# Kernel tuning notes

Measured on AMD Instinct MI355X. Metric: run time of the kernel, lower is better.

## Reference

```python
import jax, jax.numpy as jnp
import numpy as np

B, M = 512, 32          # graphs, atoms per graph
N = B * M               # 16384 nodes
F_IN, H, L = 16, 128, 2 # input feat, hidden, n interaction layers
CUTOFF = 1.0
BOX = 2.0               # side of position box -> avg degree ~16 at r=1


def _glorot(k, shape):
    fan_in = shape[-2]
    return jax.random.normal(k, shape, dtype=jnp.float32) / np.sqrt(fan_in)


def setup_inputs():
    key = jax.random.key(0)
    ks = jax.random.split(key, 12)
    return {
        "h": jax.random.normal(ks[0], (N, F_IN), dtype=jnp.float32),
        "x": jax.random.uniform(ks[1], (N, 3), dtype=jnp.float32) * BOX,
        "batch": jnp.repeat(jnp.arange(B, dtype=jnp.int32), M),
        "W_in": _glorot(ks[2], (F_IN, H)), "b_in": jnp.zeros((H,), jnp.float32),
        "We1": _glorot(ks[3], (L, 2 * H + 1, H)), "be1": jnp.zeros((L, H), jnp.float32),
        "We2": _glorot(ks[4], (L, H, H)), "be2": jnp.zeros((L, H), jnp.float32),
        "Wh1": _glorot(ks[5], (L, 2 * H, H)), "bh1": jnp.zeros((L, H), jnp.float32),
        "Wh2": _glorot(ks[6], (L, H, H)), "bh2": jnp.zeros((L, H), jnp.float32),
        "W_out": _glorot(ks[7], (H, H)), "b_out": jnp.zeros((H,), jnp.float32),
        "Wn1": _glorot(ks[8], (H, H)), "bn1": jnp.zeros((H,), jnp.float32),
        "Wn2": _glorot(ks[9], (H, 1)), "bn2": jnp.zeros((1,), jnp.float32),
    }


def reference(h, x, batch, W_in, b_in, We1, be1, We2, be2, Wh1, bh1, Wh2, bh2, W_out, b_out, Wn1, bn1, Wn2, bn2):
    # radius graph within each molecule, fixed-shape dense mask [B,M,M]
    xg = x.reshape(B, M, 3)
    diff = xg[:, :, None, :] - xg[:, None, :, :]                 # [B,M,M,3]
    d2 = jnp.sum(diff * diff, axis=-1)                            # [B,M,M]
    adj = (d2 < CUTOFF * CUTOFF) & (~jnp.eye(M, dtype=bool))      # no self-loops

    hg = (h @ W_in + b_in).reshape(B, M, H)                       # embedding_in
    for l in range(L):  # sake_conv interaction layers
        Wa, Wb, wd = We1[l, :H], We1[l, H:2 * H], We1[l, 2 * H]
        mi = jnp.einsum('bmh,hk->bmk', hg, Wa)
        mj = jnp.einsum('bmh,hk->bmk', hg, Wb)
        # edge message phi_e([h_i, h_j, ||x_i-x_j||^2])
        m = jax.nn.silu(mi[:, :, None, :] + mj[:, None, :, :] + d2[..., None] * wd + be1[l])
        m = jax.nn.silu(jnp.einsum('bijh,hk->bijk', m, We2[l]) + be2[l])
        m = jnp.where(adj[..., None], m, 0.0)
        agg = jnp.sum(m, axis=2)                                  # scatter-add over neighbors j
        # node update phi_h([h_i, m_i]) with residual
        u = jax.nn.silu(jnp.einsum('bmh,hk->bmk', hg, Wh1[l, :H])
                        + jnp.einsum('bmh,hk->bmk', agg, Wh1[l, H:]) + bh1[l])
        hg = hg + jnp.einsum('bmh,hk->bmk', u, Wh2[l]) + bh2[l]

    ho = hg.reshape(N, H) @ W_out + b_out                         # embedding_out
    e = jax.nn.silu(ho @ Wn1 + bn1) @ Wn2 + bn2                   # energy_network -> [N,1]
    out = jax.ops.segment_sum(e, batch, num_segments=B)           # per-graph energy pooling
    return out.squeeze()
```

## Files before the change

### kernel.cpp

```cpp
#include <hip/hip_runtime.h>
#include <hip/hip_bf16.h>


#define NB 512

typedef __bf16 bf16x8 __attribute__((ext_vector_type(8)));
typedef __bf16 bf16x2 __attribute__((ext_vector_type(2)));
typedef float f32x4 __attribute__((ext_vector_type(4)));

__device__ __forceinline__ unsigned short f2bf(float f) {
    unsigned int u = __float_as_uint(f);
    u = u + 0x7FFFu + ((u >> 16) & 1u);
    return (unsigned short)(u >> 16);
}
__device__ __forceinline__ unsigned int packbf(float lo, float hi) {
    bf16x2 t;
    t.x = (__bf16)lo;
    t.y = (__bf16)hi;
    return __builtin_bit_cast(unsigned int, t);
}
__device__ __forceinline__ float bflo(unsigned int u) { return __uint_as_float(u << 16); }
__device__ __forceinline__ float bfhi(unsigned int u) { return __uint_as_float(u & 0xffff0000u); }
__device__ __forceinline__ float silu_f(float v) {
    return v * __builtin_amdgcn_rcpf(1.0f + __expf(-v));
}

__global__ __launch_bounds__(256) void prep_weights(
        const float* __restrict__ We1, const float* __restrict__ We2,
        const float* __restrict__ Wh1, const float* __restrict__ Wh2,
        const float* __restrict__ W_out, const float* __restrict__ Wn1,
        unsigned short* __restrict__ ws) {
    __shared__ unsigned short t[32][33];
    const int mtx  = blockIdx.x >> 4;
    const int tile = blockIdx.x & 15;
    const int kt = tile >> 2, nt = tile & 3;
    const int tx = threadIdx.x & 31, ty = threadIdx.x >> 5;

    const int l    = (mtx < 12) ? (mtx / 6) : 0;
    const int kind = (mtx < 12) ? (mtx % 6) : (6 + (mtx - 12));
    const float* src = nullptr;
    switch (kind) {
        case 0: src = We1 + (size_t)(l*257      )*128; break;
        case 1: src = We1 + (size_t)(l*257 + 128)*128; break;
        case 2: src = We2 + (size_t)(l*128      )*128; break;
        case 3: src = Wh1 + (size_t)(l*256      )*128; break;
        case 4: src = Wh1 + (size_t)(l*256 + 128)*128; break;
        case 5: src = Wh2 + (size_t)(l*128      )*128; break;
        case 6: src = W_out; break;
        case 7: src = Wn1;  break;
    }
    #pragma unroll
    for (int r = 0; r < 4; r++) {
        int k = kt*32 + ty + r*8;
        int n = nt*32 + tx;
        t[tx][ty + r*8] = f2bf(src[(size_t)k*128 + n]);
    }
    __syncthreads();
    unsigned short* dst = ws + ((size_t)mtx << 14);
    #pragma unroll
    for (int r = 0; r < 4; r++) {
        int nl = ty + r*8;
        int n = nt*32 + nl, k = kt*32 + tx;
        dst[(size_t)n*128 + k] = t[nl][tx];
    }
}

#define MFMA16(ACC, A, B) (ACC) = __builtin_amdgcn_mfma_f32_16x16x32_bf16((A), (B), (ACC), 0, 0, 0)

__global__ __launch_bounds__(256, 2) void sake_kernel(
    const float* __restrict__ h,   const float* __restrict__ x,
    const float* __restrict__ W_in,const float* __restrict__ b_in,
    const float* __restrict__ We1, const float* __restrict__ be1,
    const float* __restrict__ be2, const float* __restrict__ bh1,
    const float* __restrict__ bh2, const float* __restrict__ b_out,
    const float* __restrict__ bn1, const float* __restrict__ Wn2,
    const float* __restrict__ bn2, const unsigned short* __restrict__ wt,
    float* __restrict__ out)
{
    __shared__ __align__(16) float          s_d2[32*32];
    __shared__ __align__(16) float          s_hg[32*129];
    __shared__ __align__(16) unsigned short s_mimj[32*264];
    __shared__ __align__(16) unsigned short s_A1[32*136];
    __shared__ __align__(16) unsigned short s_A2[32*136];
    __shared__ __align__(16) float          s_wd[128];
    __shared__ __align__(16) float          s_be2[128];
    __shared__ __align__(16) float          s_x[32*4];
    __shared__ __align__(16) float          s_ep[256];

    const int tid  = threadIdx.x;
    const int b    = blockIdx.x;
    const int w    = tid >> 6;
    const int lane = tid & 63;
    const int quad = lane >> 4;
    const int lm   = lane & 15;
    const int mt   = w & 1;
    const int ng   = w >> 1;

    if (tid < 32) {
        s_x[tid*4+0] = x[(b*32+tid)*3+0];
        s_x[tid*4+1] = x[(b*32+tid)*3+1];
        s_x[tid*4+2] = x[(b*32+tid)*3+2];
    }
    __syncthreads();
    for (int p = tid; p < 1024; p += 256) {
        int i = p >> 5, j = p & 31;
        float dx = s_x[i*4+0]-s_x[j*4+0];
        float dy = s_x[i*4+1]-s_x[j*4+1];
        float dz = s_x[i*4+2]-s_x[j*4+2];
        s_d2[p] = dx*dx + dy*dy + dz*dz;
    }
    {
        int k = tid & 127, mg = tid >> 7;
        float c0 = W_in[       k], c1 = W_in[ 128+k], c2 = W_in[ 256+k], c3 = W_in[ 384+k];
        float c4 = W_in[ 512+k], c5 = W_in[ 640+k], c6 = W_in[ 768+k], c7 = W_in[ 896+k];
        float c8 = W_in[1024+k], c9 = W_in[1152+k], c10= W_in[1280+k], c11= W_in[1408+k];
        float c12= W_in[1536+k], c13= W_in[1664+k], c14= W_in[1792+k], c15= W_in[1920+k];
        float bi = b_in[k];
        for (int rr = 0; rr < 16; rr++) {
            int m = mg*16 + rr;
            const float4* h4 = (const float4*)(h + (size_t)(b*32 + m)*16);
            float4 h0 = h4[0], h1 = h4[1], h2 = h4[2], h3 = h4[3];
            float acc = bi
                + h0.x*c0  + h0.y*c1  + h0.z*c2  + h0.w*c3
                + h1.x*c4  + h1.y*c5  + h1.z*c6  + h1.w*c7
                + h2.x*c8  + h2.y*c9  + h2.z*c10 + h2.w*c11
                + h3.x*c12 + h3.y*c13 + h3.z*c14 + h3.w*c15;
            s_hg[m*129 + k] = acc;
        }
    }
    __syncthreads();

    for (int l = 0; l < 2; l++) {
        {
            int m = tid >> 3, c = (tid & 7) * 16;
            const float* hp = &s_hg[m*129 + c];
            uint4 pa, pb;
            pa.x = packbf(hp[0],  hp[1]);  pa.y = packbf(hp[2],  hp[3]);
            pa.z = packbf(hp[4],  hp[5]);  pa.w = packbf(hp[6],  hp[7]);
            pb.x = packbf(hp[8],  hp[9]);  pb.y = packbf(hp[10], hp[11]);
            pb.z = packbf(hp[12], hp[13]); pb.w = packbf(hp[14], hp[15]);
            *(uint4*)&s_A1[m*136 + c]     = pa;
            *(uint4*)&s_A1[m*136 + c + 8] = pb;
        }
        if (tid < 128) {
            s_wd[tid]  = We1[(l*257 + 256)*128 + tid];
            s_be2[tid] = be2[l*128 + tid];
        }
        __syncthreads();

        #pragma unroll 1
        for (int t4 = 0; t4 < 8; t4++) {
            int nt = ng + t4*2;
            const unsigned short* bt = wt + (((size_t)l*6 + (nt < 8 ? 0 : 1)) << 14);
            int ncl = (nt & 7)*16 + lm;
            f32x4 acc = {0.f,0.f,0.f,0.f};
            #pragma unroll
            for (int kb = 0; kb < 4; kb++) {
                bf16x8 a  = *(const bf16x8*)&s_A1[(mt*16+lm)*136 + kb*32 + quad*8];
                bf16x8 bb = *(const bf16x8*)&bt[ncl*128 + kb*32 + quad*8];
                MFMA16(acc, a, bb);
            }
            int c = nt*16 + lm;
            float bias = (nt >= 8) ? be1[l*128 + ncl] : 0.0f;
            s_mimj[(mt*16 + quad*4 + 0)*264 + c] = f2bf(acc.x + bias);
            s_mimj[(mt*16 + quad*4 + 1)*264 + c] = f2bf(acc.y + bias);
            s_mimj[(mt*16 + quad*4 + 2)*264 + c] = f2bf(acc.z + bias);
            s_mimj[(mt*16 + quad*4 + 3)*264 + c] = f2bf(acc.w + bias);
        }
        __syncthreads();

        {
            const unsigned short* we2t = wt + (((size_t)l*6 + 2) << 14);
            const unsigned short* bbase = we2t + lm*128 + quad*8;
            bf16x8 b0 = *(const bf16x8*)(bbase      );
            bf16x8 b1 = *(const bf16x8*)(bbase +  32);
            bf16x8 b2 = *(const bf16x8*)(bbase +  64);
            bf16x8 b3 = *(const bf16x8*)(bbase +  96);
            #pragma unroll 1
            for (int ii = 0; ii < 8; ii++) {
                const int i = ii*4 + w;
                const uint4 miu0 = *(const uint4*)&s_mimj[i*264 +  0 + quad*8];
                const uint4 miu1 = *(const uint4*)&s_mimj[i*264 + 32 + quad*8];
                const uint4 miu2 = *(const uint4*)&s_mimj[i*264 + 64 + quad*8];
                const uint4 miu3 = *(const uint4*)&s_mimj[i*264 + 96 + quad*8];
                bf16x8 a00, a01, a02, a03;
                bf16x8 a10, a11, a12, a13;
#define MAKE_AF(J, KB, MIU, AF) { \
    const uint4 mju = *(const uint4*)&s_mimj[(J)*264 + 128 + (KB)*32 + quad*8]; \
    const float4 wa = *(const float4*)&s_wd[(KB)*32 + quad*8]; \
    const float4 wb = *(const float4*)&s_wd[(KB)*32 + quad*8 + 4]; \
    uint4 au; \
    au.x = packbf(silu_f(bflo(MIU.x)+bflo(mju.x)+d2v*wa.x), silu_f(bfhi(MIU.x)+bfhi(mju.x)+d2v*wa.y)); \
    au.y = packbf(silu_f(bflo(MIU.y)+bflo(mju.y)+d2v*wa.z), silu_f(bfhi(MIU.y)+bfhi(mju.y)+d2v*wa.w)); \
    au.z = packbf(silu_f(bflo(MIU.z)+bflo(mju.z)+d2v*wb.x), silu_f(bfhi(MIU.z)+bfhi(mju.z)+d2v*wb.y)); \
    au.w = packbf(silu_f(bflo(MIU.w)+bflo(mju.w)+d2v*wb.z), silu_f(bfhi(MIU.w)+bfhi(mju.w)+d2v*wb.w)); \
    AF = __builtin_bit_cast(bf16x8, au); }
                {
                    const int j = lm;
                    const float d2v = s_d2[i*32 + j];
                    MAKE_AF(j, 0, miu0, a00) MAKE_AF(j, 1, miu1, a01)
                    MAKE_AF(j, 2, miu2, a02) MAKE_AF(j, 3, miu3, a03)
                }
                {
                    const int j = 16 + lm;
                    const float d2v = s_d2[i*32 + j];
                    MAKE_AF(j, 0, miu0, a10) MAKE_AF(j, 1, miu1, a11)
                    MAKE_AF(j, 2, miu2, a12) MAKE_AF(j, 3, miu3, a13)
                }
#undef MAKE_AF
                const int jb0 = quad*4, jb1 = 16 + quad*4;
                const float mk00 = (s_d2[i*32 + jb0 + 0] < 1.0f && (jb0+0) != i) ? 1.f : 0.f;
                const float mk01 = (s_d2[i*32 + jb0 + 1] < 1.0f && (jb0+1) != i) ? 1.f : 0.f;
                const float mk02 = (s_d2[i*32 + jb0 + 2] < 1.0f && (jb0+2) != i) ? 1.f : 0.f;
                const float mk03 = (s_d2[i*32 + jb0 + 3] < 1.0f && (jb0+3) != i) ? 1.f : 0.f;
                const float mk10 = (s_d2[i*32 + jb1 + 0] < 1.0f && (jb1+0) != i) ? 1.f : 0.f;
                const float mk11 = (s_d2[i*32 + jb1 + 1] < 1.0f && (jb1+1) != i) ? 1.f : 0.f;
                const float mk12 = (s_d2[i*32 + jb1 + 2] < 1.0f && (jb1+2) != i) ? 1.f : 0.f;
                const float mk13 = (s_d2[i*32 + jb1 + 3] < 1.0f && (jb1+3) != i) ? 1.f : 0.f;

                #pragma unroll 1
                for (int nt = 0; nt < 8; nt++) {
                    const unsigned short* np = bbase + (((nt + 1) & 7) * 2048);
                    bf16x8 n0 = *(const bf16x8*)(np      );
                    bf16x8 n1 = *(const bf16x8*)(np +  32);
                    bf16x8 n2 = *(const bf16x8*)(np +  64);
                    bf16x8 n3 = *(const bf16x8*)(np +  96);
                    f32x4 ac0 = {0.f,0.f,0.f,0.f};
                    f32x4 ac1 = {0.f,0.f,0.f,0.f};
                    MFMA16(ac0, a00, b0); MFMA16(ac0, a01, b1);
                    MFMA16(ac0, a02, b2); MFMA16(ac0, a03, b3);
                    MFMA16(ac1, a10, b0); MFMA16(ac1, a11, b1);
                    MFMA16(ac1, a12, b2); MFMA16(ac1, a13, b3);
                    const float bv = s_be2[nt*16 + lm];
                    float part = mk00*silu_f(ac0.x + bv) + mk01*silu_f(ac0.y + bv)
                               + mk02*silu_f(ac0.z + bv) + mk03*silu_f(ac0.w + bv)
                               + mk10*silu_f(ac1.x + bv) + mk11*silu_f(ac1.y + bv)
                               + mk12*silu_f(ac1.z + bv) + mk13*silu_f(ac1.w + bv);
                    part += __shfl_xor(part, 16);
                    part += __shfl_xor(part, 32);
                    if (lane < 16) s_A2[i*136 + nt*16 + lane] = f2bf(part);
                    b0 = n0; b1 = n1; b2 = n2; b3 = n3;
                }
            }
        }
        __syncthreads();

        unsigned short* s_u = s_mimj;
        {
            const unsigned short* w1a = wt + (((size_t)l*6 + 3) << 14);
            const unsigned short* w1b = wt + (((size_t)l*6 + 4) << 14);
#define U_GEMM(T2) { \
    const int nt = ng + (T2)*2, ncl = nt*16 + lm; \
    f32x4 acc = {0.f,0.f,0.f,0.f}; \
    _Pragma("unroll") \
    for (int kb = 0; kb < 4; kb++) { \
        bf16x8 a  = *(const bf16x8*)&s_A1[(mt*16+lm)*136 + kb*32 + quad*8]; \
        bf16x8 bb = *(const bf16x8*)&w1a[ncl*128 + kb*32 + quad*8]; \
        MFMA16(acc, a, bb); } \
    _Pragma("unroll") \
    for (int kb = 0; kb < 4; kb++) { \
        bf16x8 a  = *(const bf16x8*)&s_A2[(mt*16+lm)*136 + kb*32 + quad*8]; \
        bf16x8 bb = *(const bf16x8*)&w1b[ncl*128 + kb*32 + quad*8]; \
        MFMA16(acc, a, bb); } \
    const float bh = bh1[l*128 + ncl]; \
    s_u[(mt*16 + quad*4 + 0)*136 + ncl] = f2bf(silu_f(acc.x + bh)); \
    s_u[(mt*16 + quad*4 + 1)*136 + ncl] = f2bf(silu_f(acc.y + bh)); \
    s_u[(mt*16 + quad*4 + 2)*136 + ncl] = f2bf(silu_f(acc.z + bh)); \
    s_u[(mt*16 + quad*4 + 3)*136 + ncl] = f2bf(silu_f(acc.w + bh)); }
            U_GEMM(0) U_GEMM(1) U_GEMM(2) U_GEMM(3)
#undef U_GEMM
        }
        __syncthreads();

        {
            const unsigned short* w2 = wt + (((size_t)l*6 + 5) << 14);
#define H_GEMM(T2) { \
    const int nt = ng + (T2)*2, ncl = nt*16 + lm; \
    f32x4 acc = {0.f,0.f,0.f,0.f}; \
    _Pragma("unroll") \
    for (int kb = 0; kb < 4; kb++) { \
        bf16x8 a  = *(const bf16x8*)&s_u[(mt*16+lm)*136 + kb*32 + quad*8]; \
        bf16x8 bb = *(const bf16x8*)&w2[ncl*128 + kb*32 + quad*8]; \
        MFMA16(acc, a, bb); } \
    const float bh = bh2[l*128 + ncl]; \
    s_hg[(mt*16 + quad*4 + 0)*129 + ncl] += acc.x + bh; \
    s_hg[(mt*16 + quad*4 + 1)*129 + ncl] += acc.y + bh; \
    s_hg[(mt*16 + quad*4 + 2)*129 + ncl] += acc.z + bh; \
    s_hg[(mt*16 + quad*4 + 3)*129 + ncl] += acc.w + bh; }
            H_GEMM(0) H_GEMM(1) H_GEMM(2) H_GEMM(3)
#undef H_GEMM
        }
        __syncthreads();
    }

    {
        int m = tid >> 3, c = (tid & 7) * 16;
        const float* hp = &s_hg[m*129 + c];
        uint4 pa, pb;
        pa.x = packbf(hp[0],  hp[1]);  pa.y = packbf(hp[2],  hp[3]);
        pa.z = packbf(hp[4],  hp[5]);  pa.w = packbf(hp[6],  hp[7]);
        pb.x = packbf(hp[8],  hp[9]);  pb.y = packbf(hp[10], hp[11]);
        pb.z = packbf(hp[12], hp[13]); pb.w = packbf(hp[14], hp[15]);
        *(uint4*)&s_A1[m*136 + c]     = pa;
        *(uint4*)&s_A1[m*136 + c + 8] = pb;
    }
    __syncthreads();
    {
        const unsigned short* wo = wt + ((size_t)12 << 14);
#define O_GEMM(T2) { \
    const int nt = ng + (T2)*2, ncl = nt*16 + lm; \
    f32x4 acc = {0.f,0.f,0.f,0.f}; \
    _Pragma("unroll") \
    for (int kb = 0; kb < 4; kb++) { \
        bf16x8 a  = *(const bf16x8*)&s_A1[(mt*16+lm)*136 + kb*32 + quad*8]; \
        bf16x8 bb = *(const bf16x8*)&wo[ncl*128 + kb*32 + quad*8]; \
        MFMA16(acc, a, bb); } \
    const float bo = b_out[ncl]; \
    s_A2[(mt*16 + quad*4 + 0)*136 + ncl] = f2bf(acc.x + bo); \
    s_A2[(mt*16 + quad*4 + 1)*136 + ncl] = f2bf(acc.y + bo); \
    s_A2[(mt*16 + quad*4 + 2)*136 + ncl] = f2bf(acc.z + bo); \
    s_A2[(mt*16 + quad*4 + 3)*136 + ncl] = f2bf(acc.w + bo); }
        O_GEMM(0) O_GEMM(1) O_GEMM(2) O_GEMM(3)
#undef O_GEMM
    }
    __syncthreads();
    float* s_g = (float*)s_mimj;
    {
        const unsigned short* wn1 = wt + ((size_t)13 << 14);
#define G_GEMM(T2) { \
    const int nt = ng + (T2)*2, ncl = nt*16 + lm; \
    f32x4 acc = {0.f,0.f,0.f,0.f}; \
    _Pragma("unroll") \
    for (int kb = 0; kb < 4; kb++) { \
        bf16x8 a  = *(const bf16x8*)&s_A2[(mt*16+lm)*136 + kb*32 + quad*8]; \
        bf16x8 bb = *(const bf16x8*)&wn1[ncl*128 + kb*32 + quad*8]; \
        MFMA16(acc, a, bb); } \
    const float bn = bn1[ncl]; \
    s_g[(mt*16 + quad*4 + 0)*129 + ncl] = silu_f(acc.x + bn); \
    s_g[(mt*16 + quad*4 + 1)*129 + ncl] = silu_f(acc.y + bn); \
    s_g[(mt*16 + quad*4 + 2)*129 + ncl] = silu_f(acc.z + bn); \
    s_g[(mt*16 + quad*4 + 3)*129 + ncl] = silu_f(acc.w + bn); }
        G_GEMM(0) G_GEMM(1) G_GEMM(2) G_GEMM(3)
#undef G_GEMM
    }
    __syncthreads();
    {
        int m = tid >> 3, s = tid & 7;
        float acc = 0.f;
        #pragma unroll
        for (int q = 0; q < 16; q++) {
            int hh = s*16 + q;
            acc += s_g[m*129 + hh] * Wn2[hh];
        }
        s_ep[tid] = acc;
    }
    __syncthreads();
    if (tid < 32) {
        float e = bn2[0];
        #pragma unroll
        for (int s = 0; s < 8; s++) e += s_ep[tid*8 + s];
        #pragma unroll
        for (int off = 16; off >= 1; off >>= 1) e += __shfl_down(e, off, 32);
        if (tid == 0) out[b] = e;
    }
}

extern "C" void kernel_launch(void* const* d_in, const int* in_sizes, int n_in,
                              void* d_out, int out_size, void* d_ws, size_t ws_size,
                              hipStream_t stream) {
    const float* h     = (const float*)d_in[0];
    const float* x     = (const float*)d_in[1];
    const float* W_in  = (const float*)d_in[3];
    const float* b_in  = (const float*)d_in[4];
    const float* We1   = (const float*)d_in[5];
    const float* be1   = (const float*)d_in[6];
    const float* We2   = (const float*)d_in[7];
    const float* be2   = (const float*)d_in[8];
    const float* Wh1   = (const float*)d_in[9];
    const float* bh1   = (const float*)d_in[10];
    const float* Wh2   = (const float*)d_in[11];
    const float* bh2   = (const float*)d_in[12];
    const float* W_out = (const float*)d_in[13];
    const float* b_out = (const float*)d_in[14];
    const float* Wn1   = (const float*)d_in[15];
    const float* bn1   = (const float*)d_in[16];
    const float* Wn2   = (const float*)d_in[17];
    const float* bn2   = (const float*)d_in[18];
    unsigned short* ws = (unsigned short*)d_ws;
    float* outp = (float*)d_out;

    prep_weights<<<14*16, 256, 0, stream>>>(We1, We2, Wh1, Wh2, W_out, Wn1, ws);
    sake_kernel<<<NB, 256, 0, stream>>>(h, x, W_in, b_in, We1, be1, be2, bh1, bh2,
                                        b_out, bn1, Wn2, bn2, ws, outp);
}
```

Measured before the change: 257.6 us.

## Compact neighbor lists to skip masked edge MFMA work

Builds a per-atom compacted list of neighbors inside the cutoff (up to 16) in shared memory. When an atom has at most 16 neighbors, the edge-message computation gathers only those neighbors into one 16-row MFMA tile instead of processing all 32 candidate j's. This halves the silu/pack and MFMA work for most atoms, falling back to the dense path otherwise. The neighbor-list build runs serially on 32 threads, adds divergence between waves, and relies on later barriers for its shared-memory writes to become visible.

Measured after the change: 256.7 us (median of 2 runs). About the same (-0.4%).

```diff
diff --git a/kernel.cpp b/kernel.cpp
--- a/kernel.cpp
+++ b/kernel.cpp
@@ -86,6 +86,8 @@
     __shared__ __align__(16) float          s_be2[128];
     __shared__ __align__(16) float          s_x[32*4];
     __shared__ __align__(16) float          s_ep[256];
+    __shared__ unsigned char s_nbr[32][16];
+    __shared__ int           s_cnt[32];
 
     const int tid  = threadIdx.x;
     const int b    = blockIdx.x;
@@ -129,6 +131,18 @@
         }
     }
     __syncthreads();
+
+    if (tid < 32) {
+        int c = 0;
+        for (int j = 0; j < 32; j++) {
+            if (s_d2[tid*32 + j] < 1.0f && j != tid) {
+                if (c < 16) s_nbr[tid][c] = (unsigned char)j;
+                c++;
+            }
+        }
+        for (int q = c; q < 16; q++) s_nbr[tid][q] = (unsigned char)tid;
+        s_cnt[tid] = c;
+    }
 
     for (int l = 0; l < 2; l++) {
         {
@@ -179,12 +193,11 @@
             #pragma unroll 1
             for (int ii = 0; ii < 8; ii++) {
                 const int i = ii*4 + w;
+                const int cnt = s_cnt[i];
                 const uint4 miu0 = *(const uint4*)&s_mimj[i*264 +  0 + quad*8];
                 const uint4 miu1 = *(const uint4*)&s_mimj[i*264 + 32 + quad*8];
                 const uint4 miu2 = *(const uint4*)&s_mimj[i*264 + 64 + quad*8];
                 const uint4 miu3 = *(const uint4*)&s_mimj[i*264 + 96 + quad*8];
-                bf16x8 a00, a01, a02, a03;
-                bf16x8 a10, a11, a12, a13;
 #define MAKE_AF(J, KB, MIU, AF) { \
     const uint4 mju = *(const uint4*)&s_mimj[(J)*264 + 128 + (KB)*32 + quad*8]; \
     const float4 wa = *(const float4*)&s_wd[(KB)*32 + quad*8]; \
@@ -195,52 +208,84 @@
     au.z = packbf(silu_f(bflo(MIU.z)+bflo(mju.z)+d2v*wb.x), silu_f(bfhi(MIU.z)+bfhi(mju.z)+d2v*wb.y)); \
     au.w = packbf(silu_f(bflo(MIU.w)+bflo(mju.w)+d2v*wb.z), silu_f(bfhi(MIU.w)+bfhi(mju.w)+d2v*wb.w)); \
     AF = __builtin_bit_cast(bf16x8, au); }
-                {
-                    const int j = lm;
+                if (cnt <= 16) {
+                    const int j = s_nbr[i][lm];
                     const float d2v = s_d2[i*32 + j];
+                    bf16x8 a00, a01, a02, a03;
                     MAKE_AF(j, 0, miu0, a00) MAKE_AF(j, 1, miu1, a01)
                     MAKE_AF(j, 2, miu2, a02) MAKE_AF(j, 3, miu3, a03)
-                }
-                {
-                    const int j = 16 + lm;
-                    const float d2v = s_d2[i*32 + j];
-                    MAKE_AF(j, 0, miu0, a10) MAKE_AF(j, 1, miu1, a11)
-                    MAKE_AF(j, 2, miu2, a12) MAKE_AF(j, 3, miu3, a13)
+                    const int jb0 = quad*4;
+                    const float mk00 = (jb0 + 0 < cnt) ? 1.f : 0.f;
+                    const float mk01 = (jb0 + 1 < cnt) ? 1.f : 0.f;
+                    const float mk02 = (jb0 + 2 < cnt) ? 1.f : 0.f;
+                    const float mk03 = (jb0 + 3 < cnt) ? 1.f : 0.f;
+                    #pragma unroll 1
+                    for (int nt = 0; nt < 8; nt++) {
+                        const unsigned short* np = bbase + (((nt + 1) & 7) * 2048);
+                        bf16x8 n0 = *(const bf16x8*)(np      );
+                        bf16x8 n1 = *(const bf16x8*)(np +  32);
+                        bf16x8 n2 = *(const bf16x8*)(np +  64);
+                        bf16x8 n3 = *(const bf16x8*)(np +  96);
+                        f32x4 ac0 = {0.f,0.f,0.f,0.f};
+                        MFMA16(ac0, a00, b0); MFMA16(ac0, a01, b1);
+                        MFMA16(ac0, a02, b2); MFMA16(ac0, a03, b3);
+                        const float bv = s_be2[nt*16 + lm];
+                        float part = mk00*silu_f(ac0.x + bv) + mk01*silu_f(ac0.y + bv)
+                                   + mk02*silu_f(ac0.z + bv) + mk03*silu_f(ac0.w + bv);
+                        part += __shfl_xor(part, 16);
+                        part += __shfl_xor(part, 32);
+                        if (lane < 16) s_A2[i*136 + nt*16 + lane] = f2bf(part);
+                        b0 = n0; b1 = n1; b2 = n2; b3 = n3;
+                    }
+                } else {
+                    bf16x8 a00, a01, a02, a03;
+                    bf16x8 a10, a11, a12, a13;
+                    {
+                        const int j = lm;
+                        const float d2v = s_d2[i*32 + j];
+                        MAKE_AF(j, 0, miu0, a00) MAKE_AF(j, 1, miu1, a01)
+                        MAKE_AF(j, 2, miu2, a02) MAKE_AF(j, 3, miu3, a03)
+                    }
+                    {
+                        const int j = 16 + lm;
+                        const float d2v = s_d2[i*32 + j];
+                        MAKE_AF(j, 0, miu0, a10) MAKE_AF(j, 1, miu1, a11)
+                        MAKE_AF(j, 2, miu2, a12) MAKE_AF(j, 3, miu3, a13)
+                    }
+                    const int jb0 = quad*4, jb1 = 16 + quad*4;
+                    const float mk00 = (s_d2[i*32 + jb0 + 0] < 1.0f && (jb0+0) != i) ? 1.f : 0.f;
+                    const float mk01 = (s_d2[i*32 + jb0 + 1] < 1.0f && (jb0+1) != i) ? 1.f : 0.f;
+                    const float mk02 = (s_d2[i*32 + jb0 + 2] < 1.0f && (jb0+2) != i) ? 1.f : 0.f;
+                    const float mk03 = (s_d2[i*32 + jb0 + 3] < 1.0f && (jb0+3) != i) ? 1.f : 0.f;
+                    const float mk10 = (s_d2[i*32 + jb1 + 0] < 1.0f && (jb1+0) != i) ? 1.f : 0.f;
+                    const float mk11 = (s_d2[i*32 + jb1 + 1] < 1.0f && (jb1+1) != i) ? 1.f : 0.f;
+                    const float mk12 = (s_d2[i*32 + jb1 + 2] < 1.0f && (jb1+2) != i) ? 1.f : 0.f;
+                    const float mk13 = (s_d2[i*32 + jb1 + 3] < 1.0f && (jb1+3) != i) ? 1.f : 0.f;
+                    #pragma unroll 1
+                    for (int nt = 0; nt < 8; nt++) {
+                        const unsigned short* np = bbase + (((nt + 1) & 7) * 2048);
+                        bf16x8 n0 = *(const bf16x8*)(np      );
+                        bf16x8 n1 = *(const bf16x8*)(np +  32);
+                        bf16x8 n2 = *(const bf16x8*)(np +  64);
+                        bf16x8 n3 = *(const bf16x8*)(np +  96);
+                        f32x4 ac0 = {0.f,0.f,0.f,0.f};
+                        f32x4 ac1 = {0.f,0.f,0.f,0.f};
+                        MFMA16(ac0, a00, b0); MFMA16(ac0, a01, b1);
+                        MFMA16(ac0, a02, b2); MFMA16(ac0, a03, b3);
+                        MFMA16(ac1, a10, b0); MFMA16(ac1, a11, b1);
+                        MFMA16(ac1, a12, b2); MFMA16(ac1, a13, b3);
+                        const float bv = s_be2[nt*16 + lm];
+                        float part = mk00*silu_f(ac0.x + bv) + mk01*silu_f(ac0.y + bv)
+                                   + mk02*silu_f(ac0.z + bv) + mk03*silu_f(ac0.w + bv)
+                                   + mk10*silu_f(ac1.x + bv) + mk11*silu_f(ac1.y + bv)
+                                   + mk12*silu_f(ac1.z + bv) + mk13*silu_f(ac1.w + bv);
+                        part += __shfl_xor(part, 16);
+                        part += __shfl_xor(part, 32);
+                        if (lane < 16) s_A2[i*136 + nt*16 + lane] = f2bf(part);
+                        b0 = n0; b1 = n1; b2 = n2; b3 = n3;
+                    }
                 }
 #undef MAKE_AF
-                const int jb0 = quad*4, jb1 = 16 + quad*4;
-                const float mk00 = (s_d2[i*32 + jb0 + 0] < 1.0f && (jb0+0) != i) ? 1.f : 0.f;
-                const float mk01 = (s_d2[i*32 + jb0 + 1] < 1.0f && (jb0+1) != i) ? 1.f : 0.f;
-                const float mk02 = (s_d2[i*32 + jb0 + 2] < 1.0f && (jb0+2) != i) ? 1.f : 0.f;
-                const float mk03 = (s_d2[i*32 + jb0 + 3] < 1.0f && (jb0+3) != i) ? 1.f : 0.f;
-                const float mk10 = (s_d2[i*32 + jb1 + 0] < 1.0f && (jb1+0) != i) ? 1.f : 0.f;
-                const float mk11 = (s_d2[i*32 + jb1 + 1] < 1.0f && (jb1+1) != i) ? 1.f : 0.f;
-                const float mk12 = (s_d2[i*32 + jb1 + 2] < 1.0f && (jb1+2) != i) ? 1.f : 0.f;
-                const float mk13 = (s_d2[i*32 + jb1 + 3] < 1.0f && (jb1+3) != i) ? 1.f : 0.f;
-
-                #pragma unroll 1
-                for (int nt = 0; nt < 8; nt++) {
-                    const unsigned short* np = bbase + (((nt + 1) & 7) * 2048);
-                    bf16x8 n0 = *(const bf16x8*)(np      );
-                    bf16x8 n1 = *(const bf16x8*)(np +  32);
-                    bf16x8 n2 = *(const bf16x8*)(np +  64);
-                    bf16x8 n3 = *(const bf16x8*)(np +  96);
-                    f32x4 ac0 = {0.f,0.f,0.f,0.f};
-                    f32x4 ac1 = {0.f,0.f,0.f,0.f};
-                    MFMA16(ac0, a00, b0); MFMA16(ac0, a01, b1);
-                    MFMA16(ac0, a02, b2); MFMA16(ac0, a03, b3);
-                    MFMA16(ac1, a10, b0); MFMA16(ac1, a11, b1);
-                    MFMA16(ac1, a12, b2); MFMA16(ac1, a13, b3);
-                    const float bv = s_be2[nt*16 + lm];
-                    float part = mk00*silu_f(ac0.x + bv) + mk01*silu_f(ac0.y + bv)
-                               + mk02*silu_f(ac0.z + bv) + mk03*silu_f(ac0.w + bv)
-                               + mk10*silu_f(ac1.x + bv) + mk11*silu_f(ac1.y + bv)
-                               + mk12*silu_f(ac1.z + bv) + mk13*silu_f(ac1.w + bv);
-                    part += __shfl_xor(part, 16);
-                    part += __shfl_xor(part, 32);
-                    if (lane < 16) s_A2[i*136 + nt*16 + lane] = f2bf(part);
-                    b0 = n0; b1 = n1; b2 = n2; b3 = n3;
-                }
             }
         }
         __syncthreads();
```
